# Kernel tuning notes

Measured on AMD Instinct MI355X. Metric: run time of the kernel, lower is better.

Reference implementation:

```python
import jax, jax.numpy as jnp
import numpy as np

N_NODES = 100000
N_EDGES = 1600000
FEATURE_DIM, CONDITION_DIM, HIDDEN_DIM, LATENT_DIM = 256, 64, 128, 64


def setup_inputs() -> dict:
    key = jax.random.key(0)
    ks = jax.random.split(key, 12)

    def glorot(k, fan_in, fan_out):
        s = np.sqrt(6.0 / (fan_in + fan_out)).astype(np.float32)
        return jax.random.uniform(k, (fan_in, fan_out), jnp.float32, -s, s)

    return {
        "feature": jax.random.normal(ks[0], (N_NODES, FEATURE_DIM), jnp.float32),
        "condition": jax.random.normal(ks[1], (N_NODES, CONDITION_DIM), jnp.float32),
        "edge_index": jax.random.randint(ks[2], (2, N_EDGES), 0, N_NODES, jnp.int64),
        "W_f2h": glorot(ks[3], FEATURE_DIM, HIDDEN_DIM),
        "b_f2h": jnp.zeros((HIDDEN_DIM,), jnp.float32),
        "W_c2h": glorot(ks[4], CONDITION_DIM, HIDDEN_DIM),
        "b_c2h": jnp.zeros((HIDDEN_DIM,), jnp.float32),
        "W_h2h": glorot(ks[5], 2 * HIDDEN_DIM, HIDDEN_DIM),
        "b_h2h": jnp.zeros((HIDDEN_DIM,), jnp.float32),
        "W_h2l": glorot(ks[6], HIDDEN_DIM, LATENT_DIM),
        "b_h2l": jnp.zeros((LATENT_DIM,), jnp.float32),
    }


def reference(feature, condition, edge_index, W_f2h, b_f2h, W_c2h, b_c2h,
              W_h2h, b_h2h, W_h2l, b_h2l):
    N = feature.shape[0]
    self_loops = jnp.arange(N, dtype=edge_index.dtype)
    src = jnp.concatenate([edge_index[0], self_loops])  # message sources (j)
    dst = jnp.concatenate([edge_index[1], self_loops])  # message targets (i)

    # symmetric GCN normalization: D^{-1/2} (A+I) D^{-1/2}
    deg = jax.ops.segment_sum(jnp.ones(dst.shape[0], feature.dtype), dst,
                              num_segments=N)
    dinv = jnp.where(deg > 0, jax.lax.rsqrt(deg), 0.0)
    norm = dinv[src] * dinv[dst]  # [E+N]

    def gcn_conv(x, W, b):
        xl = x @ W                                   # [N, out]
        msg = xl[src] * norm[:, None]                # gather + scale
        return jax.ops.segment_sum(msg, dst, num_segments=N) + b

    f2h = jnp.tanh(gcn_conv(feature, W_f2h, b_f2h))
    c2h = jnp.tanh(gcn_conv(condition, W_c2h, b_c2h))
    h = jnp.concatenate([f2h, c2h], axis=1)          # [N, 2*hidden]
    h = jnp.tanh(gcn_conv(h, W_h2h, b_h2h))
    z = gcn_conv(h, W_h2l, b_h2l)
    return z
```

## Files before the change

### kernel.cpp

```cpp
#include <hip/hip_runtime.h>
#include <cmath>
#include <cstdint>


typedef _Float16 f16;
typedef _Float16 f16x8 __attribute__((ext_vector_type(8)));
typedef _Float16 f16x4 __attribute__((ext_vector_type(4)));
typedef float f32x4 __attribute__((ext_vector_type(4)));
typedef unsigned int u32x4 __attribute__((ext_vector_type(4)));
typedef unsigned int u32x2 __attribute__((ext_vector_type(2)));

__global__ void count_rank_kernel(const int* __restrict__ dst, int* __restrict__ count,
                                  int* __restrict__ rank, int E) {
    int e = blockIdx.x * 256 + threadIdx.x;
    if (e < E) rank[e] = atomicAdd(&count[dst[e]], 1);
}

constexpr int SCAN_VPT = 8;
constexpr int SCAN_TILE = 256 * SCAN_VPT;

__global__ __launch_bounds__(256) void scan_partial_kernel(const int* __restrict__ count,
                                                           float* __restrict__ dinv,
                                                           int* __restrict__ blocksums, int N) {
    __shared__ int red[256];
    const int t = threadIdx.x;
    int base = blockIdx.x * SCAN_TILE + t * SCAN_VPT;
    int s = 0;
#pragma unroll
    for (int i = 0; i < SCAN_VPT; ++i) {
        int idx = base + i;
        if (idx < N) {
            int c = count[idx];
            dinv[idx] = rsqrtf((float)(c + 1));
            s += c;
        }
    }
    red[t] = s;
    __syncthreads();
    for (int off = 128; off > 0; off >>= 1) {
        if (t < off) red[t] += red[t + off];
        __syncthreads();
    }
    if (t == 0) blocksums[blockIdx.x] = red[0];
}

__global__ __launch_bounds__(256) void scan_final_kernel(const int* __restrict__ count,
                                                         const int* __restrict__ blocksums,
                                                         int* __restrict__ row_ptr, int N, int nb) {
    __shared__ int red[256];
    __shared__ int bs[64];
    const int t = threadIdx.x;
    if (t < 64) bs[t] = (t < nb) ? blocksums[t] : 0;
    __syncthreads();
    for (int off = 1; off < 64; off <<= 1) {
        int u = (t < 64 && t >= off) ? bs[t - off] : 0;
        __syncthreads();
        if (t < 64) bs[t] += u;
        __syncthreads();
    }
    const int myBase = (blockIdx.x > 0) ? bs[blockIdx.x - 1] : 0;

    int base = blockIdx.x * SCAN_TILE + t * SCAN_VPT;
    int vals[SCAN_VPT];
    int s = 0;
#pragma unroll
    for (int i = 0; i < SCAN_VPT; ++i) {
        int idx = base + i;
        vals[i] = (idx < N) ? count[idx] : 0;
        s += vals[i];
    }
    red[t] = s;
    __syncthreads();
    for (int off = 1; off < 256; off <<= 1) {
        int u = (t >= off) ? red[t - off] : 0;
        __syncthreads();
        red[t] += u;
        __syncthreads();
    }
    int run = red[t] - s + myBase;
#pragma unroll
    for (int i = 0; i < SCAN_VPT; ++i) {
        int idx = base + i;
        if (idx < N) {
            row_ptr[idx] = run;
            run += vals[i];
            if (idx == N - 1) row_ptr[N] = run;
        }
    }
}

__global__ void fill_kernel(const int* __restrict__ src, const int* __restrict__ dst,
                            const int* __restrict__ rank, const float* __restrict__ dinv,
                            const int* __restrict__ row_ptr, long long* __restrict__ csr, int E) {
    int e = blockIdx.x * 256 + threadIdx.x;
    if (e >= E) return;
    int s = src[e];
    int d = dst[e];
    int pos = row_ptr[d] + rank[e];
    float nrm = dinv[s] * dinv[d];
    long long v = ((long long)(unsigned)__float_as_int(nrm) << 32) | (unsigned)s;
    __builtin_nontemporal_store(v, csr + pos);
}

__device__ inline void wprep_one(const float* __restrict__ W, f16* __restrict__ hi,
                                 f16* __restrict__ lo, int M, int idx) {
    int k = idx / M, m = idx % M;
    float w = W[idx];
    f16 h = (f16)w;
    int f = ((k >> 5) * (M >> 4) + (m >> 4)) * 512 + (((k >> 3) & 3) << 7) + ((m & 15) << 3) + (k & 7);
    hi[f] = h;
    lo[f] = (f16)(w - (float)h);
}

__global__ void wprep_all_kernel(const float* __restrict__ W1, f16* h1, f16* l1,
                                 const float* __restrict__ W2, f16* h2, f16* l2,
                                 const float* __restrict__ W3, f16* h3, f16* l3,
                                 const float* __restrict__ W4, f16* h4, f16* l4,
                                 const float* __restrict__ cond, f16* __restrict__ XL, int N) {
    int b = blockIdx.x;
    int t = threadIdx.x;
    if (b < 128) {
        wprep_one(W1, h1, l1, 128, b * 256 + t);
    } else if (b < 160) {
        wprep_one(W2, h2, l2, 128, (b - 128) * 256 + t);
    } else if (b < 288) {
        wprep_one(W3, h3, l3, 128, (b - 160) * 256 + t);
    } else if (b < 320) {
        wprep_one(W4, h4, l4, 64, (b - 288) * 256 + t);
    } else {
        int i = (b - 320) * 256 + t;
        if (i < N * 16) {
            int node = i >> 4, q = i & 15;
            float4 v = ((const float4*)cond)[i];
            union { f16 h[4]; uint2 u; } p;
            p.h[0] = (f16)v.x; p.h[1] = (f16)v.y; p.h[2] = (f16)v.z; p.h[3] = (f16)v.w;
            *(uint2*)(XL + (size_t)node * 192 + 128 + q * 4) = p.u;
        }
    }
}

template <int K, int M, bool X_IS_HALF>
__global__ __launch_bounds__(256) void gemm_direct_kernel(
    const void* __restrict__ Xv, const f16* __restrict__ WFh,
    const f16* __restrict__ WFl, f16* __restrict__ out,
    int ld, int colOff, int ldx, int N) {
    constexpr int BM = 128;
    constexpr int SW = M / 4;
    constexpr int CT = SW / 16;
    constexpr int RT = BM / 16;
    constexpr int KS = K / 32;
    constexpr int MT = M / 16;

    const int tid = threadIdx.x;
    const int lane = tid & 63;
    const int wv = tid >> 6;
    const int m16 = lane & 15;
    const int quad = lane >> 4;
    const int row0 = blockIdx.x * BM;

    int xr[RT];
#pragma unroll
    for (int rt = 0; rt < RT; ++rt) {
        int r = row0 + rt * 16 + m16;
        xr[rt] = r < N ? r : N - 1;
    }

    f32x4 acc[RT][CT];
#pragma unroll
    for (int rt = 0; rt < RT; ++rt)
#pragma unroll
        for (int ct = 0; ct < CT; ++ct) acc[rt][ct] = (f32x4){0.f, 0.f, 0.f, 0.f};

    for (int ks = 0; ks < KS; ++ks) {
        const int k0 = ks * 32;
        f16x8 bh[CT], bl[CT];
#pragma unroll
        for (int ct = 0; ct < CT; ++ct) {
            const int fb = ((ks * MT + wv * CT + ct) << 9) + lane * 8;
            bh[ct] = *(const f16x8*)(WFh + fb);
            bl[ct] = *(const f16x8*)(WFl + fb);
        }
#pragma unroll
        for (int rt = 0; rt < RT; ++rt) {
            f16x8 a;
            if (X_IS_HALF) {
                a = *(const f16x8*)((const f16*)Xv + (size_t)xr[rt] * ldx + k0 + quad * 8);
            } else {
                const float* xp = (const float*)Xv + (size_t)xr[rt] * ldx + k0 + quad * 8;
                f32x4 v0 = *(const f32x4*)xp;
                f32x4 v1 = *(const f32x4*)(xp + 4);
                a[0] = (f16)v0[0]; a[1] = (f16)v0[1]; a[2] = (f16)v0[2]; a[3] = (f16)v0[3];
                a[4] = (f16)v1[0]; a[5] = (f16)v1[1]; a[6] = (f16)v1[2]; a[7] = (f16)v1[3];
            }
#pragma unroll
            for (int ct = 0; ct < CT; ++ct) {
                acc[rt][ct] = __builtin_amdgcn_mfma_f32_16x16x32_f16(a, bh[ct], acc[rt][ct], 0, 0, 0);
                acc[rt][ct] = __builtin_amdgcn_mfma_f32_16x16x32_f16(a, bl[ct], acc[rt][ct], 0, 0, 0);
            }
        }
    }

#pragma unroll
    for (int rt = 0; rt < RT; ++rt) {
#pragma unroll
        for (int r = 0; r < 4; ++r) {
            int row = row0 + rt * 16 + quad * 4 + r;
            if (row < N) {
                f16* op = out + (size_t)row * ld + colOff + wv * SW + m16;
#pragma unroll
                for (int ct = 0; ct < CT; ++ct) op[ct * 16] = (f16)acc[rt][ct][r];
            }
        }
    }
}

__global__ __launch_bounds__(256) void gemm_conv23_kernel(
    const f16* __restrict__ Bh, const f16* __restrict__ W2h, const f16* __restrict__ W2l,
    const float* __restrict__ b2, const f16* __restrict__ W3h, const f16* __restrict__ W3l,
    f16* __restrict__ outXL, int N) {
    constexpr int RT = 8, CT = 2, LP = 136;
    __shared__ f16 c2s[128 * LP];

    const int tid = threadIdx.x;
    const int lane = tid & 63;
    const int wv = tid >> 6;
    const int m16 = lane & 15;
    const int quad = lane >> 4;
    const int row0 = blockIdx.x * 128;

    int xr[RT];
#pragma unroll
    for (int rt = 0; rt < RT; ++rt) {
        int r = row0 + rt * 16 + m16;
        xr[rt] = r < N ? r : N - 1;
    }

    {
        f32x4 acc2[RT][CT];
#pragma unroll
        for (int rt = 0; rt < RT; ++rt)
#pragma unroll
            for (int ct = 0; ct < CT; ++ct) acc2[rt][ct] = (f32x4){0.f, 0.f, 0.f, 0.f};
#pragma unroll
        for (int ks = 0; ks < 2; ++ks) {
            f16x8 bh[CT], bl[CT];
#pragma unroll
            for (int ct = 0; ct < CT; ++ct) {
                const int fb = ((ks * 8 + wv * CT + ct) << 9) + lane * 8;
                bh[ct] = *(const f16x8*)(W2h + fb);
                bl[ct] = *(const f16x8*)(W2l + fb);
            }
#pragma unroll
            for (int rt = 0; rt < RT; ++rt) {
                f16x8 a = *(const f16x8*)(Bh + (size_t)xr[rt] * 256 + 128 + ks * 32 + quad * 8);
#pragma unroll
                for (int ct = 0; ct < CT; ++ct) {
                    acc2[rt][ct] = __builtin_amdgcn_mfma_f32_16x16x32_f16(a, bh[ct], acc2[rt][ct], 0, 0, 0);
                    acc2[rt][ct] = __builtin_amdgcn_mfma_f32_16x16x32_f16(a, bl[ct], acc2[rt][ct], 0, 0, 0);
                }
            }
        }
        float b2r[CT];
#pragma unroll
        for (int ct = 0; ct < CT; ++ct) b2r[ct] = b2[wv * 32 + ct * 16 + m16];
#pragma unroll
        for (int rt = 0; rt < RT; ++rt)
#pragma unroll
            for (int r = 0; r < 4; ++r) {
                int row = rt * 16 + quad * 4 + r;
#pragma unroll
                for (int ct = 0; ct < CT; ++ct)
                    c2s[row * LP + wv * 32 + ct * 16 + m16] = (f16)tanhf(acc2[rt][ct][r] + b2r[ct]);
            }
    }
    __syncthreads();

    f32x4 acc3[RT][CT];
#pragma unroll
    for (int rt = 0; rt < RT; ++rt)
#pragma unroll
        for (int ct = 0; ct < CT; ++ct) acc3[rt][ct] = (f32x4){0.f, 0.f, 0.f, 0.f};
#pragma unroll
    for (int ks = 0; ks < 8; ++ks) {
        f16x8 bh[CT], bl[CT];
#pragma unroll
        for (int ct = 0; ct < CT; ++ct) {
            const int fb = ((ks * 8 + wv * CT + ct) << 9) + lane * 8;
            bh[ct] = *(const f16x8*)(W3h + fb);
            bl[ct] = *(const f16x8*)(W3l + fb);
        }
#pragma unroll
        for (int rt = 0; rt < RT; ++rt) {
            f16x8 a;
            if (ks < 4) {
                a = *(const f16x8*)(Bh + (size_t)xr[rt] * 256 + ks * 32 + quad * 8);
            } else {
                a = *(const f16x8*)(&c2s[(rt * 16 + m16) * LP + (ks - 4) * 32 + quad * 8]);
            }
#pragma unroll
            for (int ct = 0; ct < CT; ++ct) {
                acc3[rt][ct] = __builtin_amdgcn_mfma_f32_16x16x32_f16(a, bh[ct], acc3[rt][ct], 0, 0, 0);
                acc3[rt][ct] = __builtin_amdgcn_mfma_f32_16x16x32_f16(a, bl[ct], acc3[rt][ct], 0, 0, 0);
            }
        }
    }

#pragma unroll
    for (int rt = 0; rt < RT; ++rt)
#pragma unroll
        for (int r = 0; r < 4; ++r) {
            int row = row0 + rt * 16 + quad * 4 + r;
            if (row < N) {
                f16* op = outXL + (size_t)row * 128 + wv * 32 + m16;
#pragma unroll
                for (int ct = 0; ct < CT; ++ct) op[ct * 16] = (f16)acc3[rt][ct][r];
            }
        }
}

template <int M, bool TANH, bool HAS_BIAS, bool OUT_F32>
__global__ __launch_bounds__(256) void gather_h_kernel(
    const f16* __restrict__ xl, const float* __restrict__ b,
    const float* __restrict__ dinv, const int* __restrict__ row_ptr,
    const long long* __restrict__ csr, void* __restrict__ outv,
    int ld, int colOff, int N) {
    constexpr int TPN = M / 8;
    int gid = blockIdx.x * 256 + threadIdx.x;
    int node = gid / TPN;
    int t = gid % TPN;
    if (node >= N) return;

    float di = dinv[node];
    float self = di * di;
    f16x8 x = *(const f16x8*)(xl + (size_t)node * M + t * 8);
    float acc[8];
#pragma unroll
    for (int j = 0; j < 8; ++j) acc[j] = (float)x[j] * self;
    if (HAS_BIAS) {
        float4 b0 = *(const float4*)(b + t * 8);
        float4 b1 = *(const float4*)(b + t * 8 + 4);
        acc[0] += b0.x; acc[1] += b0.y; acc[2] += b0.z; acc[3] += b0.w;
        acc[4] += b1.x; acc[5] += b1.y; acc[6] += b1.z; acc[7] += b1.w;
    }

    int p = row_ptr[node];
    const int p1 = row_ptr[node + 1];
    const int last = p1 - 1;
    long long e0 = 0, e1 = 0, e2 = 0, e3 = 0;
    if (p < p1) {
        e0 = __builtin_nontemporal_load(csr + p);
        e1 = __builtin_nontemporal_load(csr + (p + 1 < p1 ? p + 1 : last));
        e2 = __builtin_nontemporal_load(csr + (p + 2 < p1 ? p + 2 : last));
        e3 = __builtin_nontemporal_load(csr + (p + 3 < p1 ? p + 3 : last));
    }
    while (p < p1) {
        const long long c0 = e0, c1 = e1, c2 = e2, c3 = e3;
        const int pn = p + 4;
        if (pn < p1) {
            e0 = __builtin_nontemporal_load(csr + pn);
            e1 = __builtin_nontemporal_load(csr + (pn + 1 < p1 ? pn + 1 : last));
            e2 = __builtin_nontemporal_load(csr + (pn + 2 < p1 ? pn + 2 : last));
            e3 = __builtin_nontemporal_load(csr + (pn + 3 < p1 ? pn + 3 : last));
        }
        int s0 = (int)c0, s1 = (int)c1, s2 = (int)c2, s3 = (int)c3;
        float n0 = __int_as_float((int)(c0 >> 32));
        float n1 = (p + 1 < p1) ? __int_as_float((int)(c1 >> 32)) : 0.f;
        float n2 = (p + 2 < p1) ? __int_as_float((int)(c2 >> 32)) : 0.f;
        float n3 = (p + 3 < p1) ? __int_as_float((int)(c3 >> 32)) : 0.f;
        f16x8 v0 = *(const f16x8*)(xl + (size_t)s0 * M + t * 8);
        f16x8 v1 = *(const f16x8*)(xl + (size_t)s1 * M + t * 8);
        f16x8 v2 = *(const f16x8*)(xl + (size_t)s2 * M + t * 8);
        f16x8 v3 = *(const f16x8*)(xl + (size_t)s3 * M + t * 8);
#pragma unroll
        for (int j = 0; j < 8; ++j)
            acc[j] += ((float)v0[j] * n0 + (float)v1[j] * n1) +
                      ((float)v2[j] * n2 + (float)v3[j] * n3);
        p = pn;
    }

    if (TANH) {
#pragma unroll
        for (int j = 0; j < 8; ++j) acc[j] = tanhf(acc[j]);
    }

    if (OUT_F32) {
        float* op = (float*)outv + (size_t)node * ld + colOff + t * 8;
        f32x4 o0 = {acc[0], acc[1], acc[2], acc[3]};
        f32x4 o1 = {acc[4], acc[5], acc[6], acc[7]};
        __builtin_nontemporal_store(o0, (f32x4*)op);
        __builtin_nontemporal_store(o1, (f32x4*)(op + 4));
    } else {
        union { f16 h[8]; u32x4 u; } o;
#pragma unroll
        for (int j = 0; j < 8; ++j) o.h[j] = (f16)acc[j];
        __builtin_nontemporal_store(o.u, (u32x4*)((f16*)outv + (size_t)node * ld + colOff + t * 8));
    }
}

__global__ __launch_bounds__(256) void gather_fused_kernel(
    const f16* __restrict__ XL, const float* __restrict__ bA,
    const float* __restrict__ dinv, const int* __restrict__ row_ptr,
    const long long* __restrict__ csr, f16* __restrict__ out, int N) {
    int gid = blockIdx.x * 256 + threadIdx.x;
    int node = gid >> 4;
    int t = gid & 15;
    if (node >= N) return;

    float di = dinv[node];
    float self = di * di;
    const f16* base = XL + (size_t)node * 192;
    f16x8 xa = *(const f16x8*)(base + t * 8);
    f16x4 xc = *(const f16x4*)(base + 128 + t * 4);
    float accA[8], accC[4];
#pragma unroll
    for (int j = 0; j < 8; ++j) accA[j] = (float)xa[j] * self;
#pragma unroll
    for (int j = 0; j < 4; ++j) accC[j] = (float)xc[j] * self;
    {
        float4 b0 = *(const float4*)(bA + t * 8);
        float4 b1 = *(const float4*)(bA + t * 8 + 4);
        accA[0] += b0.x; accA[1] += b0.y; accA[2] += b0.z; accA[3] += b0.w;
        accA[4] += b1.x; accA[5] += b1.y; accA[6] += b1.z; accA[7] += b1.w;
    }

    int p = row_ptr[node];
    const int p1 = row_ptr[node + 1];
    const int last = p1 - 1;
    long long e0 = 0, e1 = 0, e2 = 0, e3 = 0;
    if (p < p1) {
        e0 = __builtin_nontemporal_load(csr + p);
        e1 = __builtin_nontemporal_load(csr + (p + 1 < p1 ? p + 1 : last));
        e2 = __builtin_nontemporal_load(csr + (p + 2 < p1 ? p + 2 : last));
        e3 = __builtin_nontemporal_load(csr + (p + 3 < p1 ? p + 3 : last));
    }
    while (p < p1) {
        const long long c0 = e0, c1 = e1, c2 = e2, c3 = e3;
        const int pn = p + 4;
        if (pn < p1) {
            e0 = __builtin_nontemporal_load(csr + pn);
            e1 = __builtin_nontemporal_load(csr + (pn + 1 < p1 ? pn + 1 : last));
            e2 = __builtin_nontemporal_load(csr + (pn + 2 < p1 ? pn + 2 : last));
            e3 = __builtin_nontemporal_load(csr + (pn + 3 < p1 ? pn + 3 : last));
        }
        int s0 = (int)c0, s1 = (int)c1, s2 = (int)c2, s3 = (int)c3;
        float n0 = __int_as_float((int)(c0 >> 32));
        float n1 = (p + 1 < p1) ? __int_as_float((int)(c1 >> 32)) : 0.f;
        float n2 = (p + 2 < p1) ? __int_as_float((int)(c2 >> 32)) : 0.f;
        float n3 = (p + 3 < p1) ? __int_as_float((int)(c3 >> 32)) : 0.f;
        const f16* r0 = XL + (size_t)s0 * 192;
        const f16* r1 = XL + (size_t)s1 * 192;
        const f16* r2 = XL + (size_t)s2 * 192;
        const f16* r3 = XL + (size_t)s3 * 192;
        f16x8 a0 = *(const f16x8*)(r0 + t * 8);
        f16x8 a1 = *(const f16x8*)(r1 + t * 8);
        f16x8 a2 = *(const f16x8*)(r2 + t * 8);
        f16x8 a3 = *(const f16x8*)(r3 + t * 8);
        f16x4 q0 = *(const f16x4*)(r0 + 128 + t * 4);
        f16x4 q1 = *(const f16x4*)(r1 + 128 + t * 4);
        f16x4 q2 = *(const f16x4*)(r2 + 128 + t * 4);
        f16x4 q3 = *(const f16x4*)(r3 + 128 + t * 4);
#pragma unroll
        for (int j = 0; j < 8; ++j)
            accA[j] += ((float)a0[j] * n0 + (float)a1[j] * n1) +
                       ((float)a2[j] * n2 + (float)a3[j] * n3);
#pragma unroll
        for (int j = 0; j < 4; ++j)
            accC[j] += ((float)q0[j] * n0 + (float)q1[j] * n1) +
                       ((float)q2[j] * n2 + (float)q3[j] * n3);
        p = pn;
    }

#pragma unroll
    for (int j = 0; j < 8; ++j) accA[j] = tanhf(accA[j]);

    union { f16 h[8]; u32x4 u; } oa;
#pragma unroll
    for (int j = 0; j < 8; ++j) oa.h[j] = (f16)accA[j];
    __builtin_nontemporal_store(oa.u, (u32x4*)(out + (size_t)node * 256 + t * 8));
    union { f16 h[4]; u32x2 u; } oc;
#pragma unroll
    for (int j = 0; j < 4; ++j) oc.h[j] = (f16)accC[j];
    __builtin_nontemporal_store(oc.u, (u32x2*)(out + (size_t)node * 256 + 128 + t * 4));
}

__global__ __launch_bounds__(256) void gather34_kernel(
    const f16* __restrict__ xl, const float* __restrict__ b,
    const float* __restrict__ dinv, const int* __restrict__ row_ptr,
    const long long* __restrict__ csr, const f16* __restrict__ W4h,
    const f16* __restrict__ W4l, f16* __restrict__ zpre, int N) {
    constexpr int LP = 136;
    __shared__ f16 h2s[16 * LP];
    const int tid = threadIdx.x;
    const int nloc = tid >> 4;
    const int t = tid & 15;
    const int node = blockIdx.x * 16 + nloc;
    const bool active = node < N;

    float acc[8];
    if (active) {
        float di = dinv[node];
        float self = di * di;
        f16x8 x = *(const f16x8*)(xl + (size_t)node * 128 + t * 8);
#pragma unroll
        for (int j = 0; j < 8; ++j) acc[j] = (float)x[j] * self;
        {
            float4 b0 = *(const float4*)(b + t * 8);
            float4 b1 = *(const float4*)(b + t * 8 + 4);
            acc[0] += b0.x; acc[1] += b0.y; acc[2] += b0.z; acc[3] += b0.w;
            acc[4] += b1.x; acc[5] += b1.y; acc[6] += b1.z; acc[7] += b1.w;
        }

        int p = row_ptr[node];
        const int p1 = row_ptr[node + 1];
        const int last = p1 - 1;
        long long e0 = 0, e1 = 0, e2 = 0, e3 = 0;
        if (p < p1) {
            e0 = __builtin_nontemporal_load(csr + p);
            e1 = __builtin_nontemporal_load(csr + (p + 1 < p1 ? p + 1 : last));
            e2 = __builtin_nontemporal_load(csr + (p + 2 < p1 ? p + 2 : last));
            e3 = __builtin_nontemporal_load(csr + (p + 3 < p1 ? p + 3 : last));
        }
        while (p < p1) {
            const long long c0 = e0, c1 = e1, c2 = e2, c3 = e3;
            const int pn = p + 4;
            if (pn < p1) {
                e0 = __builtin_nontemporal_load(csr + pn);
                e1 = __builtin_nontemporal_load(csr + (pn + 1 < p1 ? pn + 1 : last));
                e2 = __builtin_nontemporal_load(csr + (pn + 2 < p1 ? pn + 2 : last));
                e3 = __builtin_nontemporal_load(csr + (pn + 3 < p1 ? pn + 3 : last));
            }
            int s0 = (int)c0, s1 = (int)c1, s2 = (int)c2, s3 = (int)c3;
            float n0 = __int_as_float((int)(c0 >> 32));
            float n1 = (p + 1 < p1) ? __int_as_float((int)(c1 >> 32)) : 0.f;
            float n2 = (p + 2 < p1) ? __int_as_float((int)(c2 >> 32)) : 0.f;
            float n3 = (p + 3 < p1) ? __int_as_float((int)(c3 >> 32)) : 0.f;
            f16x8 v0 = *(const f16x8*)(xl + (size_t)s0 * 128 + t * 8);
            f16x8 v1 = *(const f16x8*)(xl + (size_t)s1 * 128 + t * 8);
            f16x8 v2 = *(const f16x8*)(xl + (size_t)s2 * 128 + t * 8);
            f16x8 v3 = *(const f16x8*)(xl + (size_t)s3 * 128 + t * 8);
#pragma unroll
            for (int j = 0; j < 8; ++j)
                acc[j] += ((float)v0[j] * n0 + (float)v1[j] * n1) +
                          ((float)v2[j] * n2 + (float)v3[j] * n3);
            p = pn;
        }

        union { f16 h[8]; u32x4 u; } o;
#pragma unroll
        for (int j = 0; j < 8; ++j) o.h[j] = (f16)tanhf(acc[j]);
        *(u32x4*)(&h2s[nloc * LP + t * 8]) = o.u;
    }
    __syncthreads();

    const int lane = tid & 63;
    const int wv = tid >> 6;
    const int m16 = lane & 15;
    const int quad = lane >> 4;

    f32x4 a4 = (f32x4){0.f, 0.f, 0.f, 0.f};
#pragma unroll
    for (int ks = 0; ks < 4; ++ks) {
        f16x8 av = *(const f16x8*)(&h2s[m16 * LP + ks * 32 + quad * 8]);
        const int fb = ((ks * 4 + wv) << 9) + lane * 8;
        f16x8 bh = *(const f16x8*)(W4h + fb);
        f16x8 bl = *(const f16x8*)(W4l + fb);
        a4 = __builtin_amdgcn_mfma_f32_16x16x32_f16(av, bh, a4, 0, 0, 0);
        a4 = __builtin_amdgcn_mfma_f32_16x16x32_f16(av, bl, a4, 0, 0, 0);
    }
#pragma unroll
    for (int r = 0; r < 4; ++r) {
        int g = blockIdx.x * 16 + quad * 4 + r;
        if (g < N) zpre[(size_t)g * 64 + wv * 16 + m16] = (f16)a4[r];
    }
}

extern "C" void kernel_launch(void* const* d_in, const int* in_sizes, int n_in,
                              void* d_out, int out_size, void* d_ws, size_t ws_size,
                              hipStream_t stream) {
    const int FD = 256;

    const float* feature   = (const float*)d_in[0];
    const float* condition = (const float*)d_in[1];
    const int*   edge      = (const int*)d_in[2];
    const float* W_f2h = (const float*)d_in[3];
    const float* b_f2h = (const float*)d_in[4];
    const float* W_c2h = (const float*)d_in[5];
    const float* b_c2h = (const float*)d_in[6];
    const float* W_h2h = (const float*)d_in[7];
    const float* b_h2h = (const float*)d_in[8];
    const float* W_h2l = (const float*)d_in[9];
    const float* b_h2l = (const float*)d_in[10];
    float* out = (float*)d_out;

    const int N = in_sizes[0] / FD;
    const int E = in_sizes[2] / 2;
    const int* src = edge;
    const int* dst = edge + E;

    float* ws_f   = (float*)d_ws;
    float* dinv   = ws_f;
    int*   count  = (int*)(ws_f + N);
    int*   rowp   = count + N;
    int*   bsums  = rowp + N + 1;
    int*   rank   = bsums + 1024;
    long long* csr = (long long*)(((uintptr_t)(rank + E) + 15) & ~(uintptr_t)15);
    f16*   XL     = (f16*)(csr + E);
    f16*   B_h    = XL + (size_t)N * 192;
    f16*   wt1h   = B_h + (size_t)N * 256;
    f16*   wt1l   = wt1h + 128 * 256;
    f16*   wt2h   = wt1l + 128 * 256;
    f16*   wt2l   = wt2h + 128 * 64;
    f16*   wt3h   = wt2l + 128 * 64;
    f16*   wt3l   = wt3h + 128 * 256;
    f16*   wt4h   = wt3l + 128 * 256;
    f16*   wt4l   = wt4h + 64 * 128;

    const int TB = 256;
    dim3 blk(TB);
    const int nScanBlocks = (N + SCAN_TILE - 1) / SCAN_TILE;
    const int condBlocks = (N * 16 + TB - 1) / TB;

    hipMemsetAsync(count, 0, (size_t)N * sizeof(int), stream);
    wprep_all_kernel<<<320 + condBlocks, blk, 0, stream>>>(
        W_f2h, wt1h, wt1l, W_c2h, wt2h, wt2l, W_h2h, wt3h, wt3l, W_h2l, wt4h, wt4l,
        condition, XL, N);

    count_rank_kernel<<<(E + TB - 1) / TB, blk, 0, stream>>>(dst, count, rank, E);
    scan_partial_kernel<<<nScanBlocks, blk, 0, stream>>>(count, dinv, bsums, N);
    scan_final_kernel<<<nScanBlocks, blk, 0, stream>>>(count, bsums, rowp, N, nScanBlocks);
    fill_kernel<<<(E + TB - 1) / TB, blk, 0, stream>>>(src, dst, rank, dinv, rowp, csr, E);

    const int gemm_grid = (N + 127) / 128;
    const int g128 = (N * 16 + TB - 1) / TB;
    const int g64  = (N * 8 + TB - 1) / TB;

    gemm_direct_kernel<256, 128, false><<<gemm_grid, blk, 0, stream>>>(
        feature, wt1h, wt1l, XL, 192, 0, 256, N);

    gather_fused_kernel<<<g128, blk, 0, stream>>>(
        XL, b_f2h, dinv, rowp, csr, B_h, N);

    gemm_conv23_kernel<<<gemm_grid, blk, 0, stream>>>(
        B_h, wt2h, wt2l, b_c2h, wt3h, wt3l, XL, N);

    gather34_kernel<<<g128, blk, 0, stream>>>(
        XL, b_h2h, dinv, rowp, csr, wt4h, wt4l, B_h, N);

    gather_h_kernel<64, false, true, true><<<g64, blk, 0, stream>>>(
        B_h, b_h2l, dinv, rowp, csr, out, 64, 0, N);
}
```

Baseline: 693.6 us.

## Use persistent grid-stride blocks for gather kernels and fold edge counting into prep

The three gather kernels now run on a fixed grid of 2048 blocks, each looping over node chunks with a grid-stride loop instead of launching one block per chunk. The aim is to cut block launch and scheduling overhead and improve load balance. The edge-degree counting is also merged into the weight/condition prep kernel, removing one launch and letting the two run side by side. Costs: gather34 gains an extra __syncthreads per chunk, and a fixed grid size may underfill or poorly balance the GPU.

```diff
diff --git a/kernel.cpp b/kernel.cpp
--- a/kernel.cpp
+++ b/kernel.cpp
@@ -10,10 +10,48 @@
 typedef unsigned int u32x4 __attribute__((ext_vector_type(4)));
 typedef unsigned int u32x2 __attribute__((ext_vector_type(2)));
 
-__global__ void count_rank_kernel(const int* __restrict__ dst, int* __restrict__ count,
-                                  int* __restrict__ rank, int E) {
-    int e = blockIdx.x * 256 + threadIdx.x;
-    if (e < E) rank[e] = atomicAdd(&count[dst[e]], 1);
+constexpr int PERSIST_BLOCKS = 2048;
+
+__device__ inline void wprep_one(const float* __restrict__ W, f16* __restrict__ hi,
+                                 f16* __restrict__ lo, int M, int idx) {
+    int k = idx / M, m = idx % M;
+    float w = W[idx];
+    f16 h = (f16)w;
+    int f = ((k >> 5) * (M >> 4) + (m >> 4)) * 512 + (((k >> 3) & 3) << 7) + ((m & 15) << 3) + (k & 7);
+    hi[f] = h;
+    lo[f] = (f16)(w - (float)h);
+}
+
+__global__ void prep_graph_kernel(const int* __restrict__ dst, int* __restrict__ count,
+                                  int* __restrict__ rank, int E, int cb,
+                                  const float* __restrict__ W1, f16* h1, f16* l1,
+                                  const float* __restrict__ W2, f16* h2, f16* l2,
+                                  const float* __restrict__ W3, f16* h3, f16* l3,
+                                  const float* __restrict__ W4, f16* h4, f16* l4,
+                                  const float* __restrict__ cond, f16* __restrict__ XL, int N) {
+    int b = blockIdx.x;
+    int t = threadIdx.x;
+    if (b < cb) {
+        int e = b * 256 + t;
+        if (e < E) rank[e] = atomicAdd(&count[dst[e]], 1);
+    } else if (b < cb + 128) {
+        wprep_one(W1, h1, l1, 128, (b - cb) * 256 + t);
+    } else if (b < cb + 160) {
+        wprep_one(W2, h2, l2, 128, (b - cb - 128) * 256 + t);
+    } else if (b < cb + 288) {
+        wprep_one(W3, h3, l3, 128, (b - cb - 160) * 256 + t);
+    } else if (b < cb + 320) {
+        wprep_one(W4, h4, l4, 64, (b - cb - 288) * 256 + t);
+    } else {
+        int i = (b - cb - 320) * 256 + t;
+        if (i < N * 16) {
+            int node = i >> 4, q = i & 15;
+            float4 v = ((const float4*)cond)[i];
+            union { f16 h[4]; uint2 u; } p;
+            p.h[0] = (f16)v.x; p.h[1] = (f16)v.y; p.h[2] = (f16)v.z; p.h[3] = (f16)v.w;
+            *(uint2*)(XL + (size_t)node * 192 + 128 + q * 4) = p.u;
+        }
+    }
 }
 
 constexpr int SCAN_VPT = 8;
@@ -102,43 +140,6 @@
     __builtin_nontemporal_store(v, csr + pos);
 }
 
-__device__ inline void wprep_one(const float* __restrict__ W, f16* __restrict__ hi,
-                                 f16* __restrict__ lo, int M, int idx) {
-    int k = idx / M, m = idx % M;
-    float w = W[idx];
-    f16 h = (f16)w;
-    int f = ((k >> 5) * (M >> 4) + (m >> 4)) * 512 + (((k >> 3) & 3) << 7) + ((m & 15) << 3) + (k & 7);
-    hi[f] = h;
-    lo[f] = (f16)(w - (float)h);
-}
-
-__global__ void wprep_all_kernel(const float* __restrict__ W1, f16* h1, f16* l1,
-                                 const float* __restrict__ W2, f16* h2, f16* l2,
-                                 const float* __restrict__ W3, f16* h3, f16* l3,
-                                 const float* __restrict__ W4, f16* h4, f16* l4,
-                                 const float* __restrict__ cond, f16* __restrict__ XL, int N) {
-    int b = blockIdx.x;
-    int t = threadIdx.x;
-    if (b < 128) {
-        wprep_one(W1, h1, l1, 128, b * 256 + t);
-    } else if (b < 160) {
-        wprep_one(W2, h2, l2, 128, (b - 128) * 256 + t);
-    } else if (b < 288) {
-        wprep_one(W3, h3, l3, 128, (b - 160) * 256 + t);
-    } else if (b < 320) {
-        wprep_one(W4, h4, l4, 64, (b - 288) * 256 + t);
-    } else {
-        int i = (b - 320) * 256 + t;
-        if (i < N * 16) {
-            int node = i >> 4, q = i & 15;
-            float4 v = ((const float4*)cond)[i];
-            union { f16 h[4]; uint2 u; } p;
-            p.h[0] = (f16)v.x; p.h[1] = (f16)v.y; p.h[2] = (f16)v.z; p.h[3] = (f16)v.w;
-            *(uint2*)(XL + (size_t)node * 192 + 128 + q * 4) = p.u;
-        }
-    }
-}
-
 template <int K, int M, bool X_IS_HALF>
 __global__ __launch_bounds__(256) void gemm_direct_kernel(
     const void* __restrict__ Xv, const f16* __restrict__ WFh,
@@ -325,75 +326,78 @@
     const long long* __restrict__ csr, void* __restrict__ outv,
     int ld, int colOff, int N) {
     constexpr int TPN = M / 8;
-    int gid = blockIdx.x * 256 + threadIdx.x;
-    int node = gid / TPN;
-    int t = gid % TPN;
-    if (node >= N) return;
-
-    float di = dinv[node];
-    float self = di * di;
-    f16x8 x = *(const f16x8*)(xl + (size_t)node * M + t * 8);
-    float acc[8];
-#pragma unroll
-    for (int j = 0; j < 8; ++j) acc[j] = (float)x[j] * self;
-    if (HAS_BIAS) {
-        float4 b0 = *(const float4*)(b + t * 8);
-        float4 b1 = *(const float4*)(b + t * 8 + 4);
-        acc[0] += b0.x; acc[1] += b0.y; acc[2] += b0.z; acc[3] += b0.w;
-        acc[4] += b1.x; acc[5] += b1.y; acc[6] += b1.z; acc[7] += b1.w;
-    }
-
-    int p = row_ptr[node];
-    const int p1 = row_ptr[node + 1];
-    const int last = p1 - 1;
-    long long e0 = 0, e1 = 0, e2 = 0, e3 = 0;
-    if (p < p1) {
-        e0 = __builtin_nontemporal_load(csr + p);
-        e1 = __builtin_nontemporal_load(csr + (p + 1 < p1 ? p + 1 : last));
-        e2 = __builtin_nontemporal_load(csr + (p + 2 < p1 ? p + 2 : last));
-        e3 = __builtin_nontemporal_load(csr + (p + 3 < p1 ? p + 3 : last));
-    }
-    while (p < p1) {
-        const long long c0 = e0, c1 = e1, c2 = e2, c3 = e3;
-        const int pn = p + 4;
-        if (pn < p1) {
-            e0 = __builtin_nontemporal_load(csr + pn);
-            e1 = __builtin_nontemporal_load(csr + (pn + 1 < p1 ? pn + 1 : last));
-            e2 = __builtin_nontemporal_load(csr + (pn + 2 < p1 ? pn + 2 : last));
-            e3 = __builtin_nontemporal_load(csr + (pn + 3 < p1 ? pn + 3 : last));
-        }
-        int s0 = (int)c0, s1 = (int)c1, s2 = (int)c2, s3 = (int)c3;
-        float n0 = __int_as_float((int)(c0 >> 32));
-        float n1 = (p + 1 < p1) ? __int_as_float((int)(c1 >> 32)) : 0.f;
-        float n2 = (p + 2 < p1) ? __int_as_float((int)(c2 >> 32)) : 0.f;
-        float n3 = (p + 3 < p1) ? __int_as_float((int)(c3 >> 32)) : 0.f;
-        f16x8 v0 = *(const f16x8*)(xl + (size_t)s0 * M + t * 8);
-        f16x8 v1 = *(const f16x8*)(xl + (size_t)s1 * M + t * 8);
-        f16x8 v2 = *(const f16x8*)(xl + (size_t)s2 * M + t * 8);
-        f16x8 v3 = *(const f16x8*)(xl + (size_t)s3 * M + t * 8);
-#pragma unroll
-        for (int j = 0; j < 8; ++j)
-            acc[j] += ((float)v0[j] * n0 + (float)v1[j] * n1) +
-                      ((float)v2[j] * n2 + (float)v3[j] * n3);
-        p = pn;
-    }
-
-    if (TANH) {
-#pragma unroll
-        for (int j = 0; j < 8; ++j) acc[j] = tanhf(acc[j]);
-    }
-
-    if (OUT_F32) {
-        float* op = (float*)outv + (size_t)node * ld + colOff + t * 8;
-        f32x4 o0 = {acc[0], acc[1], acc[2], acc[3]};
-        f32x4 o1 = {acc[4], acc[5], acc[6], acc[7]};
-        __builtin_nontemporal_store(o0, (f32x4*)op);
-        __builtin_nontemporal_store(o1, (f32x4*)(op + 4));
-    } else {
-        union { f16 h[8]; u32x4 u; } o;
-#pragma unroll
-        for (int j = 0; j < 8; ++j) o.h[j] = (f16)acc[j];
-        __builtin_nontemporal_store(o.u, (u32x4*)((f16*)outv + (size_t)node * ld + colOff + t * 8));
+    const int nch = (N * TPN + 255) / 256;
+    for (int c = blockIdx.x; c < nch; c += gridDim.x) {
+        int gid = c * 256 + threadIdx.x;
+        int node = gid / TPN;
+        int t = gid % TPN;
+        if (node >= N) continue;
+
+        float di = dinv[node];
+        float self = di * di;
+        f16x8 x = *(const f16x8*)(xl + (size_t)node * M + t * 8);
+        float acc[8];
+#pragma unroll
+        for (int j = 0; j < 8; ++j) acc[j] = (float)x[j] * self;
+        if (HAS_BIAS) {
+            float4 b0 = *(const float4*)(b + t * 8);
+            float4 b1 = *(const float4*)(b + t * 8 + 4);
+            acc[0] += b0.x; acc[1] += b0.y; acc[2] += b0.z; acc[3] += b0.w;
+            acc[4] += b1.x; acc[5] += b1.y; acc[6] += b1.z; acc[7] += b1.w;
+        }
+
+        int p = row_ptr[node];
+        const int p1 = row_ptr[node + 1];
+        const int last = p1 - 1;
+        long long e0 = 0, e1 = 0, e2 = 0, e3 = 0;
+        if (p < p1) {
+            e0 = __builtin_nontemporal_load(csr + p);
+            e1 = __builtin_nontemporal_load(csr + (p + 1 < p1 ? p + 1 : last));
+            e2 = __builtin_nontemporal_load(csr + (p + 2 < p1 ? p + 2 : last));
+            e3 = __builtin_nontemporal_load(csr + (p + 3 < p1 ? p + 3 : last));
+        }
+        while (p < p1) {
+            const long long c0 = e0, c1 = e1, c2 = e2, c3 = e3;
+            const int pn = p + 4;
+            if (pn < p1) {
+                e0 = __builtin_nontemporal_load(csr + pn);
+                e1 = __builtin_nontemporal_load(csr + (pn + 1 < p1 ? pn + 1 : last));
+                e2 = __builtin_nontemporal_load(csr + (pn + 2 < p1 ? pn + 2 : last));
+                e3 = __builtin_nontemporal_load(csr + (pn + 3 < p1 ? pn + 3 : last));
+            }
+            int s0 = (int)c0, s1 = (int)c1, s2 = (int)c2, s3 = (int)c3;
+            float n0 = __int_as_float((int)(c0 >> 32));
+            float n1 = (p + 1 < p1) ? __int_as_float((int)(c1 >> 32)) : 0.f;
+            float n2 = (p + 2 < p1) ? __int_as_float((int)(c2 >> 32)) : 0.f;
+            float n3 = (p + 3 < p1) ? __int_as_float((int)(c3 >> 32)) : 0.f;
+            f16x8 v0 = *(const f16x8*)(xl + (size_t)s0 * M + t * 8);
+            f16x8 v1 = *(const f16x8*)(xl + (size_t)s1 * M + t * 8);
+            f16x8 v2 = *(const f16x8*)(xl + (size_t)s2 * M + t * 8);
+            f16x8 v3 = *(const f16x8*)(xl + (size_t)s3 * M + t * 8);
+#pragma unroll
+            for (int j = 0; j < 8; ++j)
+                acc[j] += ((float)v0[j] * n0 + (float)v1[j] * n1) +
+                          ((float)v2[j] * n2 + (float)v3[j] * n3);
+            p = pn;
+        }
+
+        if (TANH) {
+#pragma unroll
+            for (int j = 0; j < 8; ++j) acc[j] = tanhf(acc[j]);
+        }
+
+        if (OUT_F32) {
+            float* op = (float*)outv + (size_t)node * ld + colOff + t * 8;
+            f32x4 o0 = {acc[0], acc[1], acc[2], acc[3]};
+            f32x4 o1 = {acc[4], acc[5], acc[6], acc[7]};
+            __builtin_nontemporal_store(o0, (f32x4*)op);
+            __builtin_nontemporal_store(o1, (f32x4*)(op + 4));
+        } else {
+            union { f16 h[8]; u32x4 u; } o;
+#pragma unroll
+            for (int j = 0; j < 8; ++j) o.h[j] = (f16)acc[j];
+            __builtin_nontemporal_store(o.u, (u32x4*)((f16*)outv + (size_t)node * ld + colOff + t * 8));
+        }
     }
 }
 
@@ -401,86 +405,88 @@
     const f16* __restrict__ XL, const float* __restrict__ bA,
     const float* __restrict__ dinv, const int* __restrict__ row_ptr,
     const long long* __restrict__ csr, f16* __restrict__ out, int N) {
-    int gid = blockIdx.x * 256 + threadIdx.x;
-    int node = gid >> 4;
-    int t = gid & 15;
-    if (node >= N) return;
-
-    float di = dinv[node];
-    float self = di * di;
-    const f16* base = XL + (size_t)node * 192;
-    f16x8 xa = *(const f16x8*)(base + t * 8);
-    f16x4 xc = *(const f16x4*)(base + 128 + t * 4);
-    float accA[8], accC[4];
-#pragma unroll
-    for (int j = 0; j < 8; ++j) accA[j] = (float)xa[j] * self;
-#pragma unroll
-    for (int j = 0; j < 4; ++j) accC[j] = (float)xc[j] * self;
-    {
-        float4 b0 = *(const float4*)(bA + t * 8);
-        float4 b1 = *(const float4*)(bA + t * 8 + 4);
-        accA[0] += b0.x; accA[1] += b0.y; accA[2] += b0.z; accA[3] += b0.w;
-        accA[4] += b1.x; accA[5] += b1.y; accA[6] += b1.z; accA[7] += b1.w;
-    }
-
-    int p = row_ptr[node];
-    const int p1 = row_ptr[node + 1];
-    const int last = p1 - 1;
-    long long e0 = 0, e1 = 0, e2 = 0, e3 = 0;
-    if (p < p1) {
-        e0 = __builtin_nontemporal_load(csr + p);
-        e1 = __builtin_nontemporal_load(csr + (p + 1 < p1 ? p + 1 : last));
-        e2 = __builtin_nontemporal_load(csr + (p + 2 < p1 ? p + 2 : last));
-        e3 = __builtin_nontemporal_load(csr + (p + 3 < p1 ? p + 3 : last));
-    }
-    while (p < p1) {
-        const long long c0 = e0, c1 = e1, c2 = e2, c3 = e3;
-        const int pn = p + 4;
-        if (pn < p1) {
-            e0 = __builtin_nontemporal_load(csr + pn);
-            e1 = __builtin_nontemporal_load(csr + (pn + 1 < p1 ? pn + 1 : last));
-            e2 = __builtin_nontemporal_load(csr + (pn + 2 < p1 ? pn + 2 : last));
-            e3 = __builtin_nontemporal_load(csr + (pn + 3 < p1 ? pn + 3 : last));
-        }
-        int s0 = (int)c0, s1 = (int)c1, s2 = (int)c2, s3 = (int)c3;
-        float n0 = __int_as_float((int)(c0 >> 32));
-        float n1 = (p + 1 < p1) ? __int_as_float((int)(c1 >> 32)) : 0.f;
-        float n2 = (p + 2 < p1) ? __int_as_float((int)(c2 >> 32)) : 0.f;
-        float n3 = (p + 3 < p1) ? __int_as_float((int)(c3 >> 32)) : 0.f;
-        const f16* r0 = XL + (size_t)s0 * 192;
-        const f16* r1 = XL + (size_t)s1 * 192;
-        const f16* r2 = XL + (size_t)s2 * 192;
-        const f16* r3 = XL + (size_t)s3 * 192;
-        f16x8 a0 = *(const f16x8*)(r0 + t * 8);
-        f16x8 a1 = *(const f16x8*)(r1 + t * 8);
-        f16x8 a2 = *(const f16x8*)(r2 + t * 8);
-        f16x8 a3 = *(const f16x8*)(r3 + t * 8);
-        f16x4 q0 = *(const f16x4*)(r0 + 128 + t * 4);
-        f16x4 q1 = *(const f16x4*)(r1 + 128 + t * 4);
-        f16x4 q2 = *(const f16x4*)(r2 + 128 + t * 4);
-        f16x4 q3 = *(const f16x4*)(r3 + 128 + t * 4);
-#pragma unroll
-        for (int j = 0; j < 8; ++j)
-            accA[j] += ((float)a0[j] * n0 + (float)a1[j] * n1) +
-                       ((float)a2[j] * n2 + (float)a3[j] * n3);
-#pragma unroll
-        for (int j = 0; j < 4; ++j)
-            accC[j] += ((float)q0[j] * n0 + (float)q1[j] * n1) +
-                       ((float)q2[j] * n2 + (float)q3[j] * n3);
-        p = pn;
-    }
-
-#pragma unroll
-    for (int j = 0; j < 8; ++j) accA[j] = tanhf(accA[j]);
-
-    union { f16 h[8]; u32x4 u; } oa;
-#pragma unroll
-    for (int j = 0; j < 8; ++j) oa.h[j] = (f16)accA[j];
-    __builtin_nontemporal_store(oa.u, (u32x4*)(out + (size_t)node * 256 + t * 8));
-    union { f16 h[4]; u32x2 u; } oc;
-#pragma unroll
-    for (int j = 0; j < 4; ++j) oc.h[j] = (f16)accC[j];
-    __builtin_nontemporal_store(oc.u, (u32x2*)(out + (size_t)node * 256 + 128 + t * 4));
+    const int nch = (N * 16 + 255) / 256;
+    const int t = threadIdx.x & 15;
+    for (int c = blockIdx.x; c < nch; c += gridDim.x) {
+        int node = (c * 256 + threadIdx.x) >> 4;
+        if (node >= N) continue;
+
+        float di = dinv[node];
+        float self = di * di;
+        const f16* base = XL + (size_t)node * 192;
+        f16x8 xa = *(const f16x8*)(base + t * 8);
+        f16x4 xc = *(const f16x4*)(base + 128 + t * 4);
+        float accA[8], accC[4];
+#pragma unroll
+        for (int j = 0; j < 8; ++j) accA[j] = (float)xa[j] * self;
+#pragma unroll
+        for (int j = 0; j < 4; ++j) accC[j] = (float)xc[j] * self;
+        {
+            float4 b0 = *(const float4*)(bA + t * 8);
+            float4 b1 = *(const float4*)(bA + t * 8 + 4);
+            accA[0] += b0.x; accA[1] += b0.y; accA[2] += b0.z; accA[3] += b0.w;
+            accA[4] += b1.x; accA[5] += b1.y; accA[6] += b1.z; accA[7] += b1.w;
+        }
+
+        int p = row_ptr[node];
+        const int p1 = row_ptr[node + 1];
+        const int last = p1 - 1;
+        long long e0 = 0, e1 = 0, e2 = 0, e3 = 0;
+        if (p < p1) {
+            e0 = __builtin_nontemporal_load(csr + p);
+            e1 = __builtin_nontemporal_load(csr + (p + 1 < p1 ? p + 1 : last));
+            e2 = __builtin_nontemporal_load(csr + (p + 2 < p1 ? p + 2 : last));
+            e3 = __builtin_nontemporal_load(csr + (p + 3 < p1 ? p + 3 : last));
+        }
+        while (p < p1) {
+            const long long c0 = e0, c1 = e1, c2 = e2, c3 = e3;
+            const int pn = p + 4;
+            if (pn < p1) {
+                e0 = __builtin_nontemporal_load(csr + pn);
+                e1 = __builtin_nontemporal_load(csr + (pn + 1 < p1 ? pn + 1 : last));
+                e2 = __builtin_nontemporal_load(csr + (pn + 2 < p1 ? pn + 2 : last));
+                e3 = __builtin_nontemporal_load(csr + (pn + 3 < p1 ? pn + 3 : last));
+            }
+            int s0 = (int)c0, s1 = (int)c1, s2 = (int)c2, s3 = (int)c3;
+            float n0 = __int_as_float((int)(c0 >> 32));
+            float n1 = (p + 1 < p1) ? __int_as_float((int)(c1 >> 32)) : 0.f;
+            float n2 = (p + 2 < p1) ? __int_as_float((int)(c2 >> 32)) : 0.f;
+            float n3 = (p + 3 < p1) ? __int_as_float((int)(c3 >> 32)) : 0.f;
+            const f16* r0 = XL + (size_t)s0 * 192;
+            const f16* r1 = XL + (size_t)s1 * 192;
+            const f16* r2 = XL + (size_t)s2 * 192;
+            const f16* r3 = XL + (size_t)s3 * 192;
+            f16x8 a0 = *(const f16x8*)(r0 + t * 8);
+            f16x8 a1 = *(const f16x8*)(r1 + t * 8);
+            f16x8 a2 = *(const f16x8*)(r2 + t * 8);
+            f16x8 a3 = *(const f16x8*)(r3 + t * 8);
+            f16x4 q0 = *(const f16x4*)(r0 + 128 + t * 4);
+            f16x4 q1 = *(const f16x4*)(r1 + 128 + t * 4);
+            f16x4 q2 = *(const f16x4*)(r2 + 128 + t * 4);
+            f16x4 q3 = *(const f16x4*)(r3 + 128 + t * 4);
+#pragma unroll
+            for (int j = 0; j < 8; ++j)
+                accA[j] += ((float)a0[j] * n0 + (float)a1[j] * n1) +
+                           ((float)a2[j] * n2 + (float)a3[j] * n3);
+#pragma unroll
+            for (int j = 0; j < 4; ++j)
+                accC[j] += ((float)q0[j] * n0 + (float)q1[j] * n1) +
+                           ((float)q2[j] * n2 + (float)q3[j] * n3);
+            p = pn;
+        }
+
+#pragma unroll
+        for (int j = 0; j < 8; ++j) accA[j] = tanhf(accA[j]);
+
+        union { f16 h[8]; u32x4 u; } oa;
+#pragma unroll
+        for (int j = 0; j < 8; ++j) oa.h[j] = (f16)accA[j];
+        __builtin_nontemporal_store(oa.u, (u32x4*)(out + (size_t)node * 256 + t * 8));
+        union { f16 h[4]; u32x2 u; } oc;
+#pragma unroll
+        for (int j = 0; j < 4; ++j) oc.h[j] = (f16)accC[j];
+        __builtin_nontemporal_store(oc.u, (u32x2*)(out + (size_t)node * 256 + 128 + t * 4));
+    }
 }
 
 __global__ __launch_bounds__(256) void gather34_kernel(
@@ -493,84 +499,88 @@
     const int tid = threadIdx.x;
     const int nloc = tid >> 4;
     const int t = tid & 15;
-    const int node = blockIdx.x * 16 + nloc;
-    const bool active = node < N;
-
-    float acc[8];
-    if (active) {
-        float di = dinv[node];
-        float self = di * di;
-        f16x8 x = *(const f16x8*)(xl + (size_t)node * 128 + t * 8);
-#pragma unroll
-        for (int j = 0; j < 8; ++j) acc[j] = (float)x[j] * self;
-        {
-            float4 b0 = *(const float4*)(b + t * 8);
-            float4 b1 = *(const float4*)(b + t * 8 + 4);
-            acc[0] += b0.x; acc[1] += b0.y; acc[2] += b0.z; acc[3] += b0.w;
-            acc[4] += b1.x; acc[5] += b1.y; acc[6] += b1.z; acc[7] += b1.w;
-        }
-
-        int p = row_ptr[node];
-        const int p1 = row_ptr[node + 1];
-        const int last = p1 - 1;
-        long long e0 = 0, e1 = 0, e2 = 0, e3 = 0;
-        if (p < p1) {
-            e0 = __builtin_nontemporal_load(csr + p);
-            e1 = __builtin_nontemporal_load(csr + (p + 1 < p1 ? p + 1 : last));
-            e2 = __builtin_nontemporal_load(csr + (p + 2 < p1 ? p + 2 : last));
-            e3 = __builtin_nontemporal_load(csr + (p + 3 < p1 ? p + 3 : last));
-        }
-        while (p < p1) {
-            const long long c0 = e0, c1 = e1, c2 = e2, c3 = e3;
-            const int pn = p + 4;
-            if (pn < p1) {
-                e0 = __builtin_nontemporal_load(csr + pn);
-                e1 = __builtin_nontemporal_load(csr + (pn + 1 < p1 ? pn + 1 : last));
-                e2 = __builtin_nontemporal_load(csr + (pn + 2 < p1 ? pn + 2 : last));
-                e3 = __builtin_nontemporal_load(csr + (pn + 3 < p1 ? pn + 3 : last));
-            }
-            int s0 = (int)c0, s1 = (int)c1, s2 = (int)c2, s3 = (int)c3;
-            float n0 = __int_as_float((int)(c0 >> 32));
-            float n1 = (p + 1 < p1) ? __int_as_float((int)(c1 >> 32)) : 0.f;
-            float n2 = (p + 2 < p1) ? __int_as_float((int)(c2 >> 32)) : 0.f;
-            float n3 = (p + 3 < p1) ? __int_as_float((int)(c3 >> 32)) : 0.f;
-            f16x8 v0 = *(const f16x8*)(xl + (size_t)s0 * 128 + t * 8);
-            f16x8 v1 = *(const f16x8*)(xl + (size_t)s1 * 128 + t * 8);
-            f16x8 v2 = *(const f16x8*)(xl + (size_t)s2 * 128 + t * 8);
-            f16x8 v3 = *(const f16x8*)(xl + (size_t)s3 * 128 + t * 8);
-#pragma unroll
-            for (int j = 0; j < 8; ++j)
-                acc[j] += ((float)v0[j] * n0 + (float)v1[j] * n1) +
-                          ((float)v2[j] * n2 + (float)v3[j] * n3);
-            p = pn;
-        }
-
-        union { f16 h[8]; u32x4 u; } o;
-#pragma unroll
-        for (int j = 0; j < 8; ++j) o.h[j] = (f16)tanhf(acc[j]);
-        *(u32x4*)(&h2s[nloc * LP + t * 8]) = o.u;
-    }
-    __syncthreads();
-
     const int lane = tid & 63;
     const int wv = tid >> 6;
     const int m16 = lane & 15;
     const int quad = lane >> 4;
-
-    f32x4 a4 = (f32x4){0.f, 0.f, 0.f, 0.f};
-#pragma unroll
-    for (int ks = 0; ks < 4; ++ks) {
-        f16x8 av = *(const f16x8*)(&h2s[m16 * LP + ks * 32 + quad * 8]);
-        const int fb = ((ks * 4 + wv) << 9) + lane * 8;
-        f16x8 bh = *(const f16x8*)(W4h + fb);
-        f16x8 bl = *(const f16x8*)(W4l + fb);
-        a4 = __builtin_amdgcn_mfma_f32_16x16x32_f16(av, bh, a4, 0, 0, 0);
-        a4 = __builtin_amdgcn_mfma_f32_16x16x32_f16(av, bl, a4, 0, 0, 0);
-    }
-#pragma unroll
-    for (int r = 0; r < 4; ++r) {
-        int g = blockIdx.x * 16 + quad * 4 + r;
-        if (g < N) zpre[(size_t)g * 64 + wv * 16 + m16] = (f16)a4[r];
+    const int nch = (N + 15) / 16;
+
+    for (int c = blockIdx.x; c < nch; c += gridDim.x) {
+        const int node = c * 16 + nloc;
+        const bool active = node < N;
+
+        float acc[8];
+        if (active) {
+            float di = dinv[node];
+            float self = di * di;
+            f16x8 x = *(const f16x8*)(xl + (size_t)node * 128 + t * 8);
+#pragma unroll
+            for (int j = 0; j < 8; ++j) acc[j] = (float)x[j] * self;
+            {
+                float4 b0 = *(const float4*)(b + t * 8);
+                float4 b1 = *(const float4*)(b + t * 8 + 4);
+                acc[0] += b0.x; acc[1] += b0.y; acc[2] += b0.z; acc[3] += b0.w;
+                acc[4] += b1.x; acc[5] += b1.y; acc[6] += b1.z; acc[7] += b1.w;
+            }
+
+            int p = row_ptr[node];
+            const int p1 = row_ptr[node + 1];
+            const int last = p1 - 1;
+            long long e0 = 0, e1 = 0, e2 = 0, e3 = 0;
+            if (p < p1) {
+                e0 = __builtin_nontemporal_load(csr + p);
+                e1 = __builtin_nontemporal_load(csr + (p + 1 < p1 ? p + 1 : last));
+                e2 = __builtin_nontemporal_load(csr + (p + 2 < p1 ? p + 2 : last));
+                e3 = __builtin_nontemporal_load(csr + (p + 3 < p1 ? p + 3 : last));
+            }
+            while (p < p1) {
+                const long long c0 = e0, c1 = e1, c2 = e2, c3 = e3;
+                const int pn = p + 4;
+                if (pn < p1) {
+                    e0 = __builtin_nontemporal_load(csr + pn);
+                    e1 = __builtin_nontemporal_load(csr + (pn + 1 < p1 ? pn + 1 : last));
+                    e2 = __builtin_nontemporal_load(csr + (pn + 2 < p1 ? pn + 2 : last));
+                    e3 = __builtin_nontemporal_load(csr + (pn + 3 < p1 ? pn + 3 : last));
+                }
+                int s0 = (int)c0, s1 = (int)c1, s2 = (int)c2, s3 = (int)c3;
+                float n0 = __int_as_float((int)(c0 >> 32));
+                float n1 = (p + 1 < p1) ? __int_as_float((int)(c1 >> 32)) : 0.f;
+                float n2 = (p + 2 < p1) ? __int_as_float((int)(c2 >> 32)) : 0.f;
+                float n3 = (p + 3 < p1) ? __int_as_float((int)(c3 >> 32)) : 0.f;
+                f16x8 v0 = *(const f16x8*)(xl + (size_t)s0 * 128 + t * 8);
+                f16x8 v1 = *(const f16x8*)(xl + (size_t)s1 * 128 + t * 8);
+                f16x8 v2 = *(const f16x8*)(xl + (size_t)s2 * 128 + t * 8);
+                f16x8 v3 = *(const f16x8*)(xl + (size_t)s3 * 128 + t * 8);
+#pragma unroll
+                for (int j = 0; j < 8; ++j)
+                    acc[j] += ((float)v0[j] * n0 + (float)v1[j] * n1) +
+                              ((float)v2[j] * n2 + (float)v3[j] * n3);
+                p = pn;
+            }
+
+            union { f16 h[8]; u32x4 u; } o;
+#pragma unroll
+            for (int j = 0; j < 8; ++j) o.h[j] = (f16)tanhf(acc[j]);
+            *(u32x4*)(&h2s[nloc * LP + t * 8]) = o.u;
+        }
+        __syncthreads();
+
+        f32x4 a4 = (f32x4){0.f, 0.f, 0.f, 0.f};
+#pragma unroll
+        for (int ks = 0; ks < 4; ++ks) {
+            f16x8 av = *(const f16x8*)(&h2s[m16 * LP + ks * 32 + quad * 8]);
+            const int fb = ((ks * 4 + wv) << 9) + lane * 8;
+            f16x8 bh = *(const f16x8*)(W4h + fb);
+            f16x8 bl = *(const f16x8*)(W4l + fb);
+            a4 = __builtin_amdgcn_mfma_f32_16x16x32_f16(av, bh, a4, 0, 0, 0);
+            a4 = __builtin_amdgcn_mfma_f32_16x16x32_f16(av, bl, a4, 0, 0, 0);
+        }
+#pragma unroll
+        for (int r = 0; r < 4; ++r) {
+            int g = c * 16 + quad * 4 + r;
+            if (g < N) zpre[(size_t)g * 64 + wv * 16 + m16] = (f16)a4[r];
+        }
+        __syncthreads();
     }
 }
 
@@ -618,34 +628,33 @@
     const int TB = 256;
     dim3 blk(TB);
     const int nScanBlocks = (N + SCAN_TILE - 1) / SCAN_TILE;
-    const int condBlocks = (N * 16 + TB - 1) / TB;
+    const int countBlocks = (E + TB - 1) / TB;
+    const int condBlocks  = (N * 16 + TB - 1) / TB;
 
     hipMemsetAsync(count, 0, (size_t)N * sizeof(int), stream);
-    wprep_all_kernel<<<320 + condBlocks, blk, 0, stream>>>(
+    prep_graph_kernel<<<countBlocks + 320 + condBlocks, blk, 0, stream>>>(
+        dst, count, rank, E, countBlocks,
         W_f2h, wt1h, wt1l, W_c2h, wt2h, wt2l, W_h2h, wt3h, wt3l, W_h2l, wt4h, wt4l,
         condition, XL, N);
 
-    count_rank_kernel<<<(E + TB - 1) / TB, blk, 0, stream>>>(dst, count, rank, E);
     scan_partial_kernel<<<nScanBlocks, blk, 0, stream>>>(count, dinv, bsums, N);
     scan_final_kernel<<<nScanBlocks, blk, 0, stream>>>(count, bsums, rowp, N, nScanBlocks);
     fill_kernel<<<(E + TB - 1) / TB, blk, 0, stream>>>(src, dst, rank, dinv, rowp, csr, E);
 
     const int gemm_grid = (N + 127) / 128;
-    const int g128 = (N * 16 + TB - 1) / TB;
-    const int g64  = (N * 8 + TB - 1) / TB;
 
     gemm_direct_kernel<256, 128, false><<<gemm_grid, blk, 0, stream>>>(
         feature, wt1h, wt1l, XL, 192, 0, 256, N);
 
-    gather_fused_kernel<<<g128, blk, 0, stream>>>(
+    gather_fused_kernel<<<PERSIST_BLOCKS, blk, 0, stream>>>(
         XL, b_f2h, dinv, rowp, csr, B_h, N);
 
     gemm_conv23_kernel<<<gemm_grid, blk, 0, stream>>>(
         B_h, wt2h, wt2l, b_c2h, wt3h, wt3l, XL, N);
 
-    gather34_kernel<<<g128, blk, 0, stream>>>(
+    gather34_kernel<<<PERSIST_BLOCKS, blk, 0, stream>>>(
         XL, b_h2h, dinv, rowp, csr, wt4h, wt4l, B_h, N);
 
-    gather_h_kernel<64, false, true, true><<<g64, blk, 0, stream>>>(
+    gather_h_kernel<64, false, true, true><<<PERSIST_BLOCKS, blk, 0, stream>>>(
         B_h, b_h2l, dinv, rowp, csr, out, 64, 0, N);
 }
```

Measured after the change: 692.8 us. About the same (-0.1%).
